# Kernel optimization log

Measured on AMD Instinct MI355X. Metric: run time of the kernel, lower is better.

Reference implementation:

```python
import jax, jax.numpy as jnp
import numpy as np

IN_FEATURES = 4096
OUT_FEATURES = 4096
GROUP_SIZE = 128
TOKENS = 8192


def setup_inputs() -> dict:
    key = jax.random.key(0)
    k1, k2, k3 = jax.random.split(key, 3)
    x = jax.random.normal(k1, (TOKENS, IN_FEATURES), dtype=jnp.float32)
    weight_packed = jax.random.randint(k2, (OUT_FEATURES, IN_FEATURES // 2), 0, 256, dtype=jnp.int32)
    num_groups = IN_FEATURES // GROUP_SIZE
    weight_scales = jax.random.uniform(k3, (OUT_FEATURES, num_groups), dtype=jnp.float32) * 0.02
    return {"x": x, "weight_packed": weight_packed, "weight_scales": weight_scales, "group_size": GROUP_SIZE}


def _dequantize_int4(packed, scales, group_size):
    # packed: [N, K//2] int (uint8 values); scales: [N, G]
    out_features = packed.shape[0]
    in_features = packed.shape[1] * 2
    low = (packed & 15) - 8   # even columns
    high = ((packed >> 4) & 15) - 8  # odd columns
    # interleave low/high along last axis -> [N, K]
    unpacked = jnp.stack([low, high], axis=-1).reshape(out_features, in_features)
    num_groups = in_features // group_size
    w = unpacked.reshape(out_features, num_groups, group_size).astype(scales.dtype)
    w = w * scales[:, :, None]  # per-group scale
    return w.reshape(out_features, in_features)


def reference(x, weight_packed, weight_scales, group_size):
    W = _dequantize_int4(weight_packed, weight_scales, group_size)  # [N, K]
    # nn.functional.linear: x @ W.T (bias=False)
    return jnp.einsum('tk,nk->tn', x, W)
```

## Files before the change

kernel.cpp:

```cpp
#include <hip/hip_runtime.h>
#include <cstdint>
#include <cstddef>

#define TOKENS 8192
#define IN_F   4096
#define OUT_F  4096

typedef __bf16 bf16;
typedef bf16  bf16x8 __attribute__((ext_vector_type(8)));
typedef float f32x4  __attribute__((ext_vector_type(4)));

__global__ void prep_kernel(const float* __restrict__ xin, bf16* __restrict__ xout,
                            const int* __restrict__ wp, const float* __restrict__ sc,
                            bf16* __restrict__ wout) {
    if (blockIdx.x < 16384) {
        size_t i = ((size_t)blockIdx.x * 256 + threadIdx.x) * 8;
        const float4* p = (const float4*)(xin + i);
        float4 a = p[0], b = p[1];
        bf16x8 r;
        r[0] = (bf16)a.x; r[1] = (bf16)a.y; r[2] = (bf16)a.z; r[3] = (bf16)a.w;
        r[4] = (bf16)b.x; r[5] = (bf16)b.y; r[6] = (bf16)b.z; r[7] = (bf16)b.w;
        *(bf16x8*)(xout + i) = r;
    } else {
        int t  = (blockIdx.x - 16384) * 256 + threadIdx.x;
        int j0 = t << 2;
        int n  = j0 >> 11;
        int g  = (j0 & 2047) >> 6;
        float s = sc[(n << 5) + g];
        int4 p = *(const int4*)(wp + j0);
        bf16x8 r;
        r[0] = (bf16)((float)((p.x & 15) - 8) * s);
        r[1] = (bf16)((float)(((p.x >> 4) & 15) - 8) * s);
        r[2] = (bf16)((float)((p.y & 15) - 8) * s);
        r[3] = (bf16)((float)(((p.y >> 4) & 15) - 8) * s);
        r[4] = (bf16)((float)((p.z & 15) - 8) * s);
        r[5] = (bf16)((float)(((p.z >> 4) & 15) - 8) * s);
        r[6] = (bf16)((float)((p.w & 15) - 8) * s);
        r[7] = (bf16)((float)(((p.w >> 4) & 15) - 8) * s);
        *(bf16x8*)(wout + ((size_t)j0 << 1)) = r;
    }
}


#define GLL(src, dst) __builtin_amdgcn_global_load_lds( \
    (const __attribute__((address_space(1))) void*)(src), \
    (__attribute__((address_space(3))) void*)(dst), 16, 0, 0)
#define BARX() { __builtin_amdgcn_s_barrier(); __builtin_amdgcn_sched_barrier(0); }

__global__ __launch_bounds__(512, 2)
void gemm_kernel(const bf16* __restrict__ A, const bf16* __restrict__ B,
                 float* __restrict__ C) {
    __shared__ char smem[131072] __attribute__((aligned(128)));

    const int tid  = threadIdx.x;
    const int lane = tid & 63;
    const int w    = tid >> 6;
    const int wr   = w >> 2, wc = w & 3;
    const int lrow = lane >> 3;
    const int gsw  = (lane & 7) ^ lrow;

    const int wg = ((blockIdx.x & 7) << 6) | (blockIdx.x >> 3);
    const int mt = wg >> 4;
    const int nt = wg & 15;

    const char* Abase = (const char*)A + (size_t)(mt * 256) * (IN_F * 2);
    const char* Bbase = (const char*)B + (size_t)(nt * 256) * (IN_F * 2);

    const char* gA[4];
#pragma unroll
    for (int t = 0; t < 4; ++t)
        gA[t] = Abase + (size_t)(t * 64 + w * 8 + lrow) * (IN_F * 2) + gsw * 16;
    const int rb = (w >> 2) * 64 + (w & 3) * 8;
    const int brow0 = rb, brow1 = rb + 128, brow2 = rb + 32, brow3 = rb + 160;
    const char* gB[4];
    gB[0] = Bbase + (size_t)(brow0 + lrow) * (IN_F * 2) + gsw * 16;
    gB[1] = Bbase + (size_t)(brow1 + lrow) * (IN_F * 2) + gsw * 16;
    gB[2] = Bbase + (size_t)(brow2 + lrow) * (IN_F * 2) + gsw * 16;
    gB[3] = Bbase + (size_t)(brow3 + lrow) * (IN_F * 2) + gsw * 16;

    char* const sm = smem;
#define ST_A0(b, kt) { GLL(gA[0] + (kt) * 128, sm + (b) * 65536 +     0 + w * 1024); \
                       GLL(gA[2] + (kt) * 128, sm + (b) * 65536 + 16384 + w * 1024); }
#define ST_A1(b, kt) { GLL(gA[1] + (kt) * 128, sm + (b) * 65536 +  8192 + w * 1024); \
                       GLL(gA[3] + (kt) * 128, sm + (b) * 65536 + 24576 + w * 1024); }
#define ST_B0(b, kt) { GLL(gB[0] + (kt) * 128, sm + (b) * 65536 + 32768 + brow0 * 128); \
                       GLL(gB[1] + (kt) * 128, sm + (b) * 65536 + 32768 + brow1 * 128); }
#define ST_B1(b, kt) { GLL(gB[2] + (kt) * 128, sm + (b) * 65536 + 32768 + brow2 * 128); \
                       GLL(gB[3] + (kt) * 128, sm + (b) * 65536 + 32768 + brow3 * 128); }

    const int m_lane = lane & 15, quad = lane >> 4, sw = m_lane & 7;
    const bf16x8* pA0 = (const bf16x8*)sm;
    const bf16x8* pB0 = (const bf16x8*)(sm + 32768);
    const bf16x8* pA1 = (const bf16x8*)(sm + 65536);
    const bf16x8* pB1 = (const bf16x8*)(sm + 98304);

    f32x4 acc[8][4];
#pragma unroll
    for (int i = 0; i < 8; ++i)
#pragma unroll
        for (int j = 0; j < 4; ++j) acc[i][j] = (f32x4)0.0f;

    ST_A0(0, 0); ST_B0(0, 0); ST_B1(0, 0); ST_A1(0, 0);
    ST_A0(1, 1); ST_B0(1, 1);
    asm volatile("s_waitcnt vmcnt(4)" ::: "memory");
    __builtin_amdgcn_s_barrier();

#define LDA(dst, PA, qr) \
    { _Pragma("unroll") for (int i = 0; i < 4; ++i) { \
        _Pragma("unroll") for (int kh = 0; kh < 2; ++kh) { \
            dst[i][kh] = (PA)[(wr * 128 + ((qr) * 4 + i) * 16 + m_lane) * 8 + ((kh * 4 + quad) ^ sw)]; } } }
#define LDBq(PB, qc) \
    { _Pragma("unroll") for (int j = 0; j < 2; ++j) { \
        _Pragma("unroll") for (int kh = 0; kh < 2; ++kh) { \
            bfr[(qc) * 2 + j][kh] = (PB)[(wc * 64 + ((qc) * 2 + j) * 16 + m_lane) * 8 + ((kh * 4 + quad) ^ sw)]; } } }
#define MM(afv, qr, qc) \
    { __builtin_amdgcn_s_setprio(1); \
      _Pragma("unroll") for (int i = 0; i < 4; ++i) { \
        _Pragma("unroll") for (int j = 0; j < 2; ++j) { \
          _Pragma("unroll") for (int kh = 0; kh < 2; ++kh) { \
            acc[(qr) * 4 + i][(qc) * 2 + j] = __builtin_amdgcn_mfma_f32_16x16x32_bf16( \
                afv[i][kh], bfr[(qc) * 2 + j][kh], acc[(qr) * 4 + i][(qc) * 2 + j], 0, 0, 0); } } } \
      __builtin_amdgcn_s_setprio(0); }

    for (int it = 0; it < 32; ++it) {
        const int kt0 = 2 * it;
        const int kt1 = kt0 + 1;
        const bool more = (it < 31);
        {
            bf16x8 af0[4][2], af1[4][2], bfr[4][2];
            LDA(af0, pA0, 0); LDBq(pB0, 0);
            ST_B1(1, kt1);
            BARX(); MM(af0, 0, 0);
            LDBq(pB0, 1);
            ST_A1(1, kt1);
            BARX(); MM(af0, 0, 1);
            LDA(af1, pA0, 1);
            if (more) ST_A0(0, kt0 + 2);
            BARX(); MM(af1, 1, 0);
            if (more) {
                ST_B0(0, kt0 + 2);
                asm volatile("s_waitcnt vmcnt(4)" ::: "memory");
            } else {
                asm volatile("s_waitcnt vmcnt(0)" ::: "memory");
            }
            BARX(); MM(af1, 1, 1);
        }
        {
            bf16x8 af0[4][2], af1[4][2], bfr[4][2];
            LDA(af0, pA1, 0); LDBq(pB1, 0);
            if (more) ST_B1(0, kt1 + 1);
            BARX(); MM(af0, 0, 0);
            LDBq(pB1, 1);
            if (more) ST_A1(0, kt1 + 1);
            BARX(); MM(af0, 0, 1);
            LDA(af1, pA1, 1);
            if (more) ST_A0(1, kt1 + 2);
            BARX(); MM(af1, 1, 0);
            if (more) {
                ST_B0(1, kt1 + 2);
                asm volatile("s_waitcnt vmcnt(4)" ::: "memory");
            }
            BARX(); MM(af1, 1, 1);
        }
    }

    const size_t crow0 = (size_t)(mt * 256 + wr * 128 + quad * 4) * OUT_F
                       + (size_t)(nt * 256 + wc * 64 + m_lane);
#pragma unroll
    for (int i = 0; i < 8; ++i)
#pragma unroll
        for (int r = 0; r < 4; ++r) {
            float* cp = C + crow0 + (size_t)(i * 16 + r) * OUT_F;
#pragma unroll
            for (int j = 0; j < 4; ++j) cp[j * 16] = acc[i][j][r];
        }
}

__global__ void naive_kernel(const float* __restrict__ x, const int* __restrict__ wp,
                             const float* __restrict__ sc, float* __restrict__ out) {
    int o = blockIdx.x * 256 + threadIdx.x;
    int t = o >> 12, n = o & 4095;
    const float* xr = x + (size_t)t * IN_F;
    const int*   wr2 = wp + (size_t)n * (IN_F / 2);
    float acc = 0.f;
    for (int g = 0; g < 32; ++g) {
        float s = sc[n * 32 + g];
        float part = 0.f;
        for (int j = 0; j < 64; ++j) {
            int p = wr2[g * 64 + j];
            part += xr[g * 128 + 2 * j]     * (float)((p & 15) - 8);
            part += xr[g * 128 + 2 * j + 1] * (float)(((p >> 4) & 15) - 8);
        }
        acc += part * s;
    }
    out[o] = acc;
}

extern "C" void kernel_launch(void* const* d_in, const int* in_sizes, int n_in,
                              void* d_out, int out_size, void* d_ws, size_t ws_size,
                              hipStream_t stream) {
    const float* x  = (const float*)d_in[0];
    const int*   wp = (const int*)d_in[1];
    const float* sc = (const float*)d_in[2];
    float* out = (float*)d_out;

    const size_t xb_bytes = (size_t)TOKENS * IN_F * 2;
    const size_t wb_bytes = (size_t)OUT_F * IN_F * 2;

    if (ws_size >= xb_bytes + wb_bytes) {
        bf16* xb = (bf16*)d_ws;
        bf16* wb = (bf16*)((char*)d_ws + xb_bytes);
        prep_kernel<<<dim3(16384 + 8192), dim3(256), 0, stream>>>(x, xb, wp, sc, wb);
        gemm_kernel<<<dim3((TOKENS / 256) * (OUT_F / 256)), dim3(512), 0, stream>>>(xb, wb, out);
    } else {
        naive_kernel<<<dim3((TOKENS * OUT_F) / 256), dim3(256), 0, stream>>>(x, wp, sc, out);
    }
}
```

Measured before the change: 444.3 us.

## Switch GEMM to 32x32x16 MFMA tiles and grid-stride the prep kernel

```diff
diff --git a/kernel.cpp b/kernel.cpp
--- a/kernel.cpp
+++ b/kernel.cpp
@@ -7,22 +7,24 @@
 #define OUT_F  4096
 
 typedef __bf16 bf16;
-typedef bf16  bf16x8 __attribute__((ext_vector_type(8)));
-typedef float f32x4  __attribute__((ext_vector_type(4)));
+typedef bf16  bf16x8  __attribute__((ext_vector_type(8)));
+typedef float f32x16  __attribute__((ext_vector_type(16)));
 
 __global__ void prep_kernel(const float* __restrict__ xin, bf16* __restrict__ xout,
                             const int* __restrict__ wp, const float* __restrict__ sc,
                             bf16* __restrict__ wout) {
-    if (blockIdx.x < 16384) {
-        size_t i = ((size_t)blockIdx.x * 256 + threadIdx.x) * 8;
-        const float4* p = (const float4*)(xin + i);
+    const int nth = gridDim.x * 256;
+    const int t0  = blockIdx.x * 256 + threadIdx.x;
+    for (int i = t0; i < TOKENS * IN_F / 8; i += nth) {
+        size_t off = (size_t)i * 8;
+        const float4* p = (const float4*)(xin + off);
         float4 a = p[0], b = p[1];
         bf16x8 r;
         r[0] = (bf16)a.x; r[1] = (bf16)a.y; r[2] = (bf16)a.z; r[3] = (bf16)a.w;
         r[4] = (bf16)b.x; r[5] = (bf16)b.y; r[6] = (bf16)b.z; r[7] = (bf16)b.w;
-        *(bf16x8*)(xout + i) = r;
-    } else {
-        int t  = (blockIdx.x - 16384) * 256 + threadIdx.x;
+        *(bf16x8*)(xout + off) = r;
+    }
+    for (int t = t0; t < OUT_F * IN_F / 8; t += nth) {
         int j0 = t << 2;
         int n  = j0 >> 11;
         int g  = (j0 & 2047) >> 6;
@@ -88,38 +90,36 @@
 #define ST_B1(b, kt) { GLL(gB[2] + (kt) * 128, sm + (b) * 65536 + 32768 + brow2 * 128); \
                        GLL(gB[3] + (kt) * 128, sm + (b) * 65536 + 32768 + brow3 * 128); }
 
-    const int m_lane = lane & 15, quad = lane >> 4, sw = m_lane & 7;
+    const int l31 = lane & 31, lhi = lane >> 5, sw7 = lane & 7;
     const bf16x8* pA0 = (const bf16x8*)sm;
     const bf16x8* pB0 = (const bf16x8*)(sm + 32768);
     const bf16x8* pA1 = (const bf16x8*)(sm + 65536);
     const bf16x8* pB1 = (const bf16x8*)(sm + 98304);
 
-    f32x4 acc[8][4];
-#pragma unroll
-    for (int i = 0; i < 8; ++i)
-#pragma unroll
-        for (int j = 0; j < 4; ++j) acc[i][j] = (f32x4)0.0f;
+    f32x16 acc[4][2];
+#pragma unroll
+    for (int i = 0; i < 4; ++i)
+#pragma unroll
+        for (int j = 0; j < 2; ++j) acc[i][j] = (f32x16)0.0f;
 
     ST_A0(0, 0); ST_B0(0, 0); ST_B1(0, 0); ST_A1(0, 0);
     ST_A0(1, 1); ST_B0(1, 1);
     asm volatile("s_waitcnt vmcnt(4)" ::: "memory");
     __builtin_amdgcn_s_barrier();
 
-#define LDA(dst, PA, qr) \
-    { _Pragma("unroll") for (int i = 0; i < 4; ++i) { \
-        _Pragma("unroll") for (int kh = 0; kh < 2; ++kh) { \
-            dst[i][kh] = (PA)[(wr * 128 + ((qr) * 4 + i) * 16 + m_lane) * 8 + ((kh * 4 + quad) ^ sw)]; } } }
-#define LDBq(PB, qc) \
-    { _Pragma("unroll") for (int j = 0; j < 2; ++j) { \
-        _Pragma("unroll") for (int kh = 0; kh < 2; ++kh) { \
-            bfr[(qc) * 2 + j][kh] = (PB)[(wc * 64 + ((qc) * 2 + j) * 16 + m_lane) * 8 + ((kh * 4 + quad) ^ sw)]; } } }
-#define MM(afv, qr, qc) \
+#define LDA32(dst, PA, qr) \
+    { _Pragma("unroll") for (int mi = 0; mi < 2; ++mi) { \
+        _Pragma("unroll") for (int ks = 0; ks < 4; ++ks) { \
+            dst[mi][ks] = (PA)[(wr * 128 + (qr) * 64 + mi * 32 + l31) * 8 + ((ks * 2 + lhi) ^ sw7)]; } } }
+#define LDB32(PB, nj) \
+    { _Pragma("unroll") for (int ks = 0; ks < 4; ++ks) { \
+        bfr[nj][ks] = (PB)[(wc * 64 + (nj) * 32 + l31) * 8 + ((ks * 2 + lhi) ^ sw7)]; } }
+#define MM32(afv, qr, nj) \
     { __builtin_amdgcn_s_setprio(1); \
-      _Pragma("unroll") for (int i = 0; i < 4; ++i) { \
-        _Pragma("unroll") for (int j = 0; j < 2; ++j) { \
-          _Pragma("unroll") for (int kh = 0; kh < 2; ++kh) { \
-            acc[(qr) * 4 + i][(qc) * 2 + j] = __builtin_amdgcn_mfma_f32_16x16x32_bf16( \
-                afv[i][kh], bfr[(qc) * 2 + j][kh], acc[(qr) * 4 + i][(qc) * 2 + j], 0, 0, 0); } } } \
+      _Pragma("unroll") for (int ks = 0; ks < 4; ++ks) { \
+        _Pragma("unroll") for (int mi = 0; mi < 2; ++mi) { \
+            acc[(qr) * 2 + mi][nj] = __builtin_amdgcn_mfma_f32_32x32x16_bf16( \
+                afv[mi][ks], bfr[nj][ks], acc[(qr) * 2 + mi][nj], 0, 0, 0); } } \
       __builtin_amdgcn_s_setprio(0); }
 
     for (int it = 0; it < 32; ++it) {
@@ -127,52 +127,55 @@
         const int kt1 = kt0 + 1;
         const bool more = (it < 31);
         {
-            bf16x8 af0[4][2], af1[4][2], bfr[4][2];
-            LDA(af0, pA0, 0); LDBq(pB0, 0);
+            bf16x8 af0[2][4], af1[2][4], bfr[2][4];
+            LDA32(af0, pA0, 0); LDB32(pB0, 0);
             ST_B1(1, kt1);
-            BARX(); MM(af0, 0, 0);
-            LDBq(pB0, 1);
+            BARX(); MM32(af0, 0, 0);
+            LDB32(pB0, 1);
             ST_A1(1, kt1);
-            BARX(); MM(af0, 0, 1);
-            LDA(af1, pA0, 1);
+            BARX(); MM32(af0, 0, 1);
+            LDA32(af1, pA0, 1);
             if (more) ST_A0(0, kt0 + 2);
-            BARX(); MM(af1, 1, 0);
+            BARX(); MM32(af1, 1, 0);
             if (more) {
                 ST_B0(0, kt0 + 2);
                 asm volatile("s_waitcnt vmcnt(4)" ::: "memory");
             } else {
                 asm volatile("s_waitcnt vmcnt(0)" ::: "memory");
             }
-            BARX(); MM(af1, 1, 1);
+            BARX(); MM32(af1, 1, 1);
         }
         {
-            bf16x8 af0[4][2], af1[4][2], bfr[4][2];
-            LDA(af0, pA1, 0); LDBq(pB1, 0);
+            bf16x8 af0[2][4], af1[2][4], bfr[2][4];
+            LDA32(af0, pA1, 0); LDB32(pB1, 0);
             if (more) ST_B1(0, kt1 + 1);
-            BARX(); MM(af0, 0, 0);
-            LDBq(pB1, 1);
+            BARX(); MM32(af0, 0, 0);
+            LDB32(pB1, 1);
             if (more) ST_A1(0, kt1 + 1);
-            BARX(); MM(af0, 0, 1);
-            LDA(af1, pA1, 1);
+            BARX(); MM32(af0, 0, 1);
+            LDA32(af1, pA1, 1);
             if (more) ST_A0(1, kt1 + 2);
-            BARX(); MM(af1, 1, 0);
+            BARX(); MM32(af1, 1, 0);
             if (more) {
                 ST_B0(1, kt1 + 2);
                 asm volatile("s_waitcnt vmcnt(4)" ::: "memory");
             }
-            BARX(); MM(af1, 1, 1);
-        }
-    }
-
-    const size_t crow0 = (size_t)(mt * 256 + wr * 128 + quad * 4) * OUT_F
-                       + (size_t)(nt * 256 + wc * 64 + m_lane);
-#pragma unroll
-    for (int i = 0; i < 8; ++i)
-#pragma unroll
-        for (int r = 0; r < 4; ++r) {
-            float* cp = C + crow0 + (size_t)(i * 16 + r) * OUT_F;
-#pragma unroll
-            for (int j = 0; j < 4; ++j) cp[j * 16] = acc[i][j][r];
+            BARX(); MM32(af1, 1, 1);
+        }
+    }
+
+    const size_t cbase = (size_t)(mt * 256 + wr * 128 + 4 * lhi) * OUT_F
+                       + (size_t)(nt * 256 + wc * 64 + l31);
+#pragma unroll
+    for (int t = 0; t < 4; ++t)
+#pragma unroll
+        for (int nj = 0; nj < 2; ++nj) {
+            float* cp = C + cbase + (size_t)(t * 32) * OUT_F + nj * 32;
+#pragma unroll
+            for (int rq = 0; rq < 4; ++rq)
+#pragma unroll
+                for (int rr = 0; rr < 4; ++rr)
+                    cp[(size_t)(8 * rq + rr) * OUT_F] = acc[t][nj][rq * 4 + rr];
         }
 }
 
@@ -210,7 +213,7 @@
     if (ws_size >= xb_bytes + wb_bytes) {
         bf16* xb = (bf16*)d_ws;
         bf16* wb = (bf16*)((char*)d_ws + xb_bytes);
-        prep_kernel<<<dim3(16384 + 8192), dim3(256), 0, stream>>>(x, xb, wp, sc, wb);
+        prep_kernel<<<dim3(2048), dim3(256), 0, stream>>>(x, xb, wp, sc, wb);
         gemm_kernel<<<dim3((TOKENS / 256) * (OUT_F / 256)), dim3(512), 0, stream>>>(xb, wb, out);
     } else {
         naive_kernel<<<dim3((TOKENS * OUT_F) / 256), dim3(256), 0, stream>>>(x, wp, sc, out);
```

Result: slower. 491.9 us (+10.7%).

## Use four waves with 128x128 per-wave tiles and prefetch LDS fragments across barriers

Applied to the files above, without the earlier changes.

```diff
diff --git a/kernel.cpp b/kernel.cpp
--- a/kernel.cpp
+++ b/kernel.cpp
@@ -47,7 +47,7 @@
     (__attribute__((address_space(3))) void*)(dst), 16, 0, 0)
 #define BARX() { __builtin_amdgcn_s_barrier(); __builtin_amdgcn_sched_barrier(0); }
 
-__global__ __launch_bounds__(512, 2)
+__global__ __launch_bounds__(256, 1)
 void gemm_kernel(const bf16* __restrict__ A, const bf16* __restrict__ B,
                  float* __restrict__ C) {
     __shared__ char smem[131072] __attribute__((aligned(128)));
@@ -55,7 +55,7 @@
     const int tid  = threadIdx.x;
     const int lane = tid & 63;
     const int w    = tid >> 6;
-    const int wr   = w >> 2, wc = w & 3;
+    const int wr   = w >> 1, wc = w & 1;
     const int lrow = lane >> 3;
     const int gsw  = (lane & 7) ^ lrow;
 
@@ -66,27 +66,24 @@
     const char* Abase = (const char*)A + (size_t)(mt * 256) * (IN_F * 2);
     const char* Bbase = (const char*)B + (size_t)(nt * 256) * (IN_F * 2);
 
-    const char* gA[4];
-#pragma unroll
-    for (int t = 0; t < 4; ++t)
-        gA[t] = Abase + (size_t)(t * 64 + w * 8 + lrow) * (IN_F * 2) + gsw * 16;
-    const int rb = (w >> 2) * 64 + (w & 3) * 8;
-    const int brow0 = rb, brow1 = rb + 128, brow2 = rb + 32, brow3 = rb + 160;
-    const char* gB[4];
-    gB[0] = Bbase + (size_t)(brow0 + lrow) * (IN_F * 2) + gsw * 16;
-    gB[1] = Bbase + (size_t)(brow1 + lrow) * (IN_F * 2) + gsw * 16;
-    gB[2] = Bbase + (size_t)(brow2 + lrow) * (IN_F * 2) + gsw * 16;
-    gB[3] = Bbase + (size_t)(brow3 + lrow) * (IN_F * 2) + gsw * 16;
+    const char* gA[4][2]; const char* gB[4][2];
+#pragma unroll
+    for (int q = 0; q < 4; ++q)
+#pragma unroll
+        for (int i = 0; i < 2; ++i) {
+            gA[q][i] = Abase + (size_t)(q * 64 + w * 16 + i * 8 + lrow) * (IN_F * 2) + gsw * 16;
+            gB[q][i] = Bbase + (size_t)(q * 64 + w * 16 + i * 8 + lrow) * (IN_F * 2) + gsw * 16;
+        }
 
     char* const sm = smem;
-#define ST_A0(b, kt) { GLL(gA[0] + (kt) * 128, sm + (b) * 65536 +     0 + w * 1024); \
-                       GLL(gA[2] + (kt) * 128, sm + (b) * 65536 + 16384 + w * 1024); }
-#define ST_A1(b, kt) { GLL(gA[1] + (kt) * 128, sm + (b) * 65536 +  8192 + w * 1024); \
-                       GLL(gA[3] + (kt) * 128, sm + (b) * 65536 + 24576 + w * 1024); }
-#define ST_B0(b, kt) { GLL(gB[0] + (kt) * 128, sm + (b) * 65536 + 32768 + brow0 * 128); \
-                       GLL(gB[1] + (kt) * 128, sm + (b) * 65536 + 32768 + brow1 * 128); }
-#define ST_B1(b, kt) { GLL(gB[2] + (kt) * 128, sm + (b) * 65536 + 32768 + brow2 * 128); \
-                       GLL(gB[3] + (kt) * 128, sm + (b) * 65536 + 32768 + brow3 * 128); }
+#define ST_Aq(b, q, kt) { GLL(gA[q][0] + (kt) * 128, sm + (b) * 65536 + (q) * 8192 + w * 2048); \
+                          GLL(gA[q][1] + (kt) * 128, sm + (b) * 65536 + (q) * 8192 + w * 2048 + 1024); }
+#define ST_Bq(b, q, kt) { GLL(gB[q][0] + (kt) * 128, sm + (b) * 65536 + 32768 + (q) * 8192 + w * 2048); \
+                          GLL(gB[q][1] + (kt) * 128, sm + (b) * 65536 + 32768 + (q) * 8192 + w * 2048 + 1024); }
+#define ST_A0(b, kt) { ST_Aq(b, 0, kt); ST_Aq(b, 2, kt); }
+#define ST_A1(b, kt) { ST_Aq(b, 1, kt); ST_Aq(b, 3, kt); }
+#define ST_B0(b, kt) { ST_Bq(b, 0, kt); ST_Bq(b, 2, kt); }
+#define ST_B1(b, kt) { ST_Bq(b, 1, kt); ST_Bq(b, 3, kt); }
 
     const int m_lane = lane & 15, quad = lane >> 4, sw = m_lane & 7;
     const bf16x8* pA0 = (const bf16x8*)sm;
@@ -94,85 +91,86 @@
     const bf16x8* pA1 = (const bf16x8*)(sm + 65536);
     const bf16x8* pB1 = (const bf16x8*)(sm + 98304);
 
-    f32x4 acc[8][4];
+    f32x4 acc[8][8];
 #pragma unroll
     for (int i = 0; i < 8; ++i)
 #pragma unroll
-        for (int j = 0; j < 4; ++j) acc[i][j] = (f32x4)0.0f;
+        for (int j = 0; j < 8; ++j) acc[i][j] = (f32x4)0.0f;
 
     ST_A0(0, 0); ST_B0(0, 0); ST_B1(0, 0); ST_A1(0, 0);
     ST_A0(1, 1); ST_B0(1, 1);
-    asm volatile("s_waitcnt vmcnt(4)" ::: "memory");
+    asm volatile("s_waitcnt vmcnt(8)" ::: "memory");
     __builtin_amdgcn_s_barrier();
 
 #define LDA(dst, PA, qr) \
     { _Pragma("unroll") for (int i = 0; i < 4; ++i) { \
         _Pragma("unroll") for (int kh = 0; kh < 2; ++kh) { \
             dst[i][kh] = (PA)[(wr * 128 + ((qr) * 4 + i) * 16 + m_lane) * 8 + ((kh * 4 + quad) ^ sw)]; } } }
-#define LDBq(PB, qc) \
-    { _Pragma("unroll") for (int j = 0; j < 2; ++j) { \
+#define LDB(dst, PB, qc) \
+    { _Pragma("unroll") for (int j = 0; j < 4; ++j) { \
         _Pragma("unroll") for (int kh = 0; kh < 2; ++kh) { \
-            bfr[(qc) * 2 + j][kh] = (PB)[(wc * 64 + ((qc) * 2 + j) * 16 + m_lane) * 8 + ((kh * 4 + quad) ^ sw)]; } } }
-#define MM(afv, qr, qc) \
+            dst[j][kh] = (PB)[(wc * 128 + ((qc) * 4 + j) * 16 + m_lane) * 8 + ((kh * 4 + quad) ^ sw)]; } } }
+#define MM(afv, bv, qr, qc) \
     { __builtin_amdgcn_s_setprio(1); \
       _Pragma("unroll") for (int i = 0; i < 4; ++i) { \
-        _Pragma("unroll") for (int j = 0; j < 2; ++j) { \
+        _Pragma("unroll") for (int j = 0; j < 4; ++j) { \
           _Pragma("unroll") for (int kh = 0; kh < 2; ++kh) { \
-            acc[(qr) * 4 + i][(qc) * 2 + j] = __builtin_amdgcn_mfma_f32_16x16x32_bf16( \
-                afv[i][kh], bfr[(qc) * 2 + j][kh], acc[(qr) * 4 + i][(qc) * 2 + j], 0, 0, 0); } } } \
+            acc[(qr) * 4 + i][(qc) * 4 + j] = __builtin_amdgcn_mfma_f32_16x16x32_bf16( \
+                afv[i][kh], bv[j][kh], acc[(qr) * 4 + i][(qc) * 4 + j], 0, 0, 0); } } } \
       __builtin_amdgcn_s_setprio(0); }
+
+    bf16x8 af0[4][2], af1[4][2], bq0[4][2], bq1[4][2];
+    LDA(af0, pA0, 0); LDB(bq0, pB0, 0);
 
     for (int it = 0; it < 32; ++it) {
         const int kt0 = 2 * it;
         const int kt1 = kt0 + 1;
         const bool more = (it < 31);
         {
-            bf16x8 af0[4][2], af1[4][2], bfr[4][2];
-            LDA(af0, pA0, 0); LDBq(pB0, 0);
+            LDB(bq1, pB0, 1);
             ST_B1(1, kt1);
-            BARX(); MM(af0, 0, 0);
-            LDBq(pB0, 1);
+            BARX(); MM(af0, bq0, 0, 0);
+            LDA(af1, pA0, 1);
             ST_A1(1, kt1);
-            BARX(); MM(af0, 0, 1);
-            LDA(af1, pA0, 1);
+            BARX(); MM(af0, bq1, 0, 1);
             if (more) ST_A0(0, kt0 + 2);
-            BARX(); MM(af1, 1, 0);
+            BARX(); MM(af1, bq0, 1, 0);
             if (more) {
                 ST_B0(0, kt0 + 2);
-                asm volatile("s_waitcnt vmcnt(4)" ::: "memory");
+                asm volatile("s_waitcnt vmcnt(8)" ::: "memory");
             } else {
                 asm volatile("s_waitcnt vmcnt(0)" ::: "memory");
             }
-            BARX(); MM(af1, 1, 1);
+            LDA(af0, pA1, 0); LDB(bq0, pB1, 0);
+            BARX(); MM(af1, bq1, 1, 1);
         }
         {
-            bf16x8 af0[4][2], af1[4][2], bfr[4][2];
-            LDA(af0, pA1, 0); LDBq(pB1, 0);
+            LDB(bq1, pB1, 1);
             if (more) ST_B1(0, kt1 + 1);
-            BARX(); MM(af0, 0, 0);
-            LDBq(pB1, 1);
+            BARX(); MM(af0, bq0, 0, 0);
+            LDA(af1, pA1, 1);
             if (more) ST_A1(0, kt1 + 1);
-            BARX(); MM(af0, 0, 1);
-            LDA(af1, pA1, 1);
+            BARX(); MM(af0, bq1, 0, 1);
             if (more) ST_A0(1, kt1 + 2);
-            BARX(); MM(af1, 1, 0);
+            BARX(); MM(af1, bq0, 1, 0);
             if (more) {
                 ST_B0(1, kt1 + 2);
-                asm volatile("s_waitcnt vmcnt(4)" ::: "memory");
+                asm volatile("s_waitcnt vmcnt(8)" ::: "memory");
+                LDA(af0, pA0, 0); LDB(bq0, pB0, 0);
             }
-            BARX(); MM(af1, 1, 1);
+            BARX(); MM(af1, bq1, 1, 1);
         }
     }
 
     const size_t crow0 = (size_t)(mt * 256 + wr * 128 + quad * 4) * OUT_F
-                       + (size_t)(nt * 256 + wc * 64 + m_lane);
+                       + (size_t)(nt * 256 + wc * 128 + m_lane);
 #pragma unroll
     for (int i = 0; i < 8; ++i)
 #pragma unroll
         for (int r = 0; r < 4; ++r) {
             float* cp = C + crow0 + (size_t)(i * 16 + r) * OUT_F;
 #pragma unroll
-            for (int j = 0; j < 4; ++j) cp[j * 16] = acc[i][j][r];
+            for (int j = 0; j < 8; ++j) cp[j * 16] = acc[i][j][r];
         }
 }
 
@@ -211,7 +209,7 @@
         bf16* xb = (bf16*)d_ws;
         bf16* wb = (bf16*)((char*)d_ws + xb_bytes);
         prep_kernel<<<dim3(16384 + 8192), dim3(256), 0, stream>>>(x, xb, wp, sc, wb);
-        gemm_kernel<<<dim3((TOKENS / 256) * (OUT_F / 256)), dim3(512), 0, stream>>>(xb, wb, out);
+        gemm_kernel<<<dim3((TOKENS / 256) * (OUT_F / 256)), dim3(256), 0, stream>>>(xb, wb, out);
     } else {
         naive_kernel<<<dim3((TOKENS * OUT_F) / 256), dim3(256), 0, stream>>>(x, wp, sc, out);
     }
```

Measured after the change: 551.1 us. 1.24x slower.
